# Kernel tuning notes

Hardware: AMD Instinct MI355X
Metric: run time of the kernel (lower is better)

## Reference

```python
import jax, jax.numpy as jnp
import numpy as np

EMBED_DIM = 512
NUM_HEADS = 8
HEAD_DIM = EMBED_DIM // NUM_HEADS
SHIFT_INIT = 5.0
EPS = 1e-6


def setup_inputs() -> dict:
    key = jax.random.key(0)
    ks = jax.random.split(key, 8)
    L, N, E = 2048, 4, EMBED_DIM
    query = jax.random.normal(ks[0], (L, N, E), dtype=jnp.float32)
    k_in = jax.random.normal(ks[1], (L, N, E), dtype=jnp.float32)
    v_in = jax.random.normal(ks[2], (L, N, E), dtype=jnp.float32)
    # MultiheadAttention packed projections
    in_proj_weight = jax.random.normal(ks[3], (3 * E, E), dtype=jnp.float32) / np.sqrt(E)
    in_proj_bias = jnp.zeros((3 * E,), dtype=jnp.float32)
    out_proj_weight = jax.random.normal(ks[4], (E, E), dtype=jnp.float32) / np.sqrt(E)
    out_proj_bias = jnp.zeros((E,), dtype=jnp.float32)
    # GeM parameters: p ~ N(1, 0.02), shift = 5
    p = 1.0 + 0.02 * jax.random.normal(ks[5], (E,), dtype=jnp.float32)
    shift = jnp.full((E,), SHIFT_INIT, dtype=jnp.float32)
    return {
        "query": query, "key": k_in, "value": v_in,
        "in_proj_weight": in_proj_weight, "in_proj_bias": in_proj_bias,
        "out_proj_weight": out_proj_weight, "out_proj_bias": out_proj_bias,
        "p": p, "shift": shift,
    }


def reference(query, key, value, in_proj_weight, in_proj_bias,
              out_proj_weight, out_proj_bias, p, shift):
    L, N, E = query.shape
    H, D = NUM_HEADS, HEAD_DIM
    w_q, w_k, w_v = jnp.split(in_proj_weight, 3, axis=0)   # each (E, E)
    b_q, b_k, b_v = jnp.split(in_proj_bias, 3, axis=0)

    def proj(x, w, b):
        # (L, N, E) -> (N, H, L, D)
        y = x @ w.T + b
        return y.reshape(L, N, H, D).transpose(1, 2, 0, 3)

    q = proj(query, w_q, b_q)
    k = proj(key, w_k, b_k)
    v = proj(value, w_v, b_v)

    scale = 1.0 / np.sqrt(D)
    scores = jnp.einsum('nhld,nhsd->nhls', q, k) * scale   # (N,H,L,S)
    attn = jax.nn.softmax(scores, axis=-1)

    # GeM pooling of values: shift -> power p -> weighted mean -> inverse power -> unshift
    p_h = p.reshape(H, D)[None, :, None, :]                # (1,H,1,D)
    shift_h = shift.reshape(H, D)[None, :, None, :]
    v_pos = jnp.maximum(v + shift_h, EPS)                  # keep base positive
    pooled = jnp.einsum('nhls,nhsd->nhld', attn, v_pos ** p_h)
    out_h = jnp.maximum(pooled, EPS) ** (1.0 / p_h) - shift_h  # (N,H,L,D)

    out = out_h.transpose(2, 0, 1, 3).reshape(L, N, E)     # back to (L,N,E)
    out = out @ out_proj_weight.T + out_proj_bias
    return out
```

## Files before the change

kernel.cpp:

```cpp
#include <hip/hip_runtime.h>
#include <hip/hip_bf16.h>

#define E_DIM 512
#define N_BATCH 4
#define L_SEQ 2048
#define N_HEADS 8
#define H_DIM 64
#define N_ROWS (L_SEQ * N_BATCH)
#define EPS_F 1e-6f
#define SC_Q 0.18033688f

typedef __attribute__((ext_vector_type(8))) short bf16x8;
typedef __attribute__((ext_vector_type(8))) _Float16 f16x8;
typedef __attribute__((ext_vector_type(4))) float f32x4;
typedef __attribute__((ext_vector_type(16))) float f32x16;

__device__ __forceinline__ void split2(float f, __hip_bfloat16& h, __hip_bfloat16& l) {
  h = __float2bfloat16(f);
  l = __float2bfloat16(f - __bfloat162float(h));
}

__device__ __forceinline__ unsigned int packf16(float a, float b) {
  union { _Float16 h[2]; unsigned int u; } c;
  c.h[0] = (_Float16)a;
  c.h[1] = (_Float16)b;
  return c.u;
}

__global__ __launch_bounds__(256) void wconv_kernel(
    const float* __restrict__ wio, const float* __restrict__ wo,
    __hip_bfloat16* __restrict__ wiohi, __hip_bfloat16* __restrict__ wiolo,
    __hip_bfloat16* __restrict__ wohi, __hip_bfloat16* __restrict__ wolo) {
  const int g = blockIdx.x * 256 + threadIdx.x;
  const float* src;
  __hip_bfloat16 *dh, *dl;
  int i;
  if (g < 196608) { src = wio; dh = wiohi; dl = wiolo; i = g * 4; }
  else            { src = wo;  dh = wohi;  dl = wolo;  i = (g - 196608) * 4; }
  const float4 f = *(const float4*)(src + i);
  alignas(8) __hip_bfloat16 h[4], l[4];
  split2(f.x, h[0], l[0]); split2(f.y, h[1], l[1]);
  split2(f.z, h[2], l[2]); split2(f.w, h[3], l[3]);
  *(uint2*)(dh + i) = *(const uint2*)h;
  *(uint2*)(dl + i) = *(const uint2*)l;
}

__global__ __launch_bounds__(256, 3) void proj_qkv_kernel(
    const float* __restrict__ xq, const float* __restrict__ xk,
    const float* __restrict__ xv, const __hip_bfloat16* __restrict__ whi,
    const float* __restrict__ bias, const float* __restrict__ pw,
    const float* __restrict__ sw,
    _Float16* __restrict__ qbuf, _Float16* __restrict__ kbuf,
    float* __restrict__ ubuf) {
  __shared__ __hip_bfloat16 Xh[128][40];
  __shared__ __hip_bfloat16 Xl[128][40];
  __shared__ __hip_bfloat16 Wh[128][40];
  const int z = blockIdx.z;
  const int row0 = blockIdx.x * 128;
  const int col0 = blockIdx.y * 128;
  const float* __restrict__ xsrc = (z == 0) ? xq : (z == 1) ? xk : xv;
  const int tid = threadIdx.x;
  const int lane = tid & 63;
  const int wv = tid >> 6;
  const int lidx = lane & 15;
  const int quad = lane >> 4;
  const int srow = tid >> 1;
  const int scol = (tid & 1) * 16;

  f32x4 acc[2][8];
#pragma unroll
  for (int rt = 0; rt < 2; ++rt)
#pragma unroll
    for (int ct = 0; ct < 8; ++ct) acc[rt][ct] = (f32x4){0.f, 0.f, 0.f, 0.f};

  const int ar0 = wv * 32 + lidx;

  for (int kt = 0; kt < 16; ++kt) {
    const int k0 = kt * 32;
    {
      const float* xp = xsrc + (size_t)(row0 + srow) * E_DIM + k0 + scol;
      float f[16];
      *(float4*)&f[0]  = ((const float4*)xp)[0];
      *(float4*)&f[4]  = ((const float4*)xp)[1];
      *(float4*)&f[8]  = ((const float4*)xp)[2];
      *(float4*)&f[12] = ((const float4*)xp)[3];
      alignas(16) __hip_bfloat16 hi[16], lo[16];
#pragma unroll
      for (int j = 0; j < 16; ++j) split2(f[j], hi[j], lo[j]);
      *(uint4*)&Xh[srow][scol]     = ((const uint4*)hi)[0];
      *(uint4*)&Xh[srow][scol + 8] = ((const uint4*)hi)[1];
      *(uint4*)&Xl[srow][scol]     = ((const uint4*)lo)[0];
      *(uint4*)&Xl[srow][scol + 8] = ((const uint4*)lo)[1];
    }
    {
      const size_t wof = (size_t)(z * E_DIM + col0 + srow) * E_DIM + k0 + scol;
      *(uint4*)&Wh[srow][scol]     = ((const uint4*)(whi + wof))[0];
      *(uint4*)&Wh[srow][scol + 8] = ((const uint4*)(whi + wof))[1];
    }
    __syncthreads();

    const bf16x8 ah0 = *(const bf16x8*)&Xh[ar0][quad * 8];
    const bf16x8 ah1 = *(const bf16x8*)&Xh[ar0 + 16][quad * 8];
    const bf16x8 al0 = *(const bf16x8*)&Xl[ar0][quad * 8];
    const bf16x8 al1 = *(const bf16x8*)&Xl[ar0 + 16][quad * 8];
#pragma unroll
    for (int ct = 0; ct < 8; ++ct) {
      const bf16x8 bh = *(const bf16x8*)&Wh[ct * 16 + lidx][quad * 8];
      acc[0][ct] = __builtin_amdgcn_mfma_f32_16x16x32_bf16(ah0, bh, acc[0][ct], 0, 0, 0);
      acc[0][ct] = __builtin_amdgcn_mfma_f32_16x16x32_bf16(al0, bh, acc[0][ct], 0, 0, 0);
      acc[1][ct] = __builtin_amdgcn_mfma_f32_16x16x32_bf16(ah1, bh, acc[1][ct], 0, 0, 0);
      acc[1][ct] = __builtin_amdgcn_mfma_f32_16x16x32_bf16(al1, bh, acc[1][ct], 0, 0, 0);
    }
    __syncthreads();
  }

  if (z < 2) {
    _Float16* __restrict__ dst = (z == 0) ? qbuf : kbuf;
    const float scale = (z == 0) ? SC_Q : 1.0f;
    float bv[8];
#pragma unroll
    for (int ct = 0; ct < 8; ++ct) bv[ct] = bias[z * E_DIM + col0 + ct * 16 + lidx];
#pragma unroll
    for (int rt = 0; rt < 2; ++rt)
#pragma unroll
      for (int ct = 0; ct < 8; ++ct) {
        const int e = col0 + ct * 16 + lidx;
        const int h = e >> 6, d = e & 63;
#pragma unroll
        for (int reg = 0; reg < 4; ++reg) {
          const int R = row0 + wv * 32 + rt * 16 + quad * 4 + reg;
          const int lpos = R >> 2, nb = R & 3;
          dst[(((size_t)nb * N_HEADS + h) * L_SEQ + lpos) * H_DIM + d] =
              (_Float16)((acc[rt][ct][reg] + bv[ct]) * scale);
        }
      }
  } else {
    float bv[8], pv[8], sv[8];
#pragma unroll
    for (int ct = 0; ct < 8; ++ct) {
      const int e = col0 + ct * 16 + lidx;
      bv[ct] = bias[2 * E_DIM + e]; pv[ct] = pw[e]; sv[ct] = sw[e];
    }
#pragma unroll
    for (int rt = 0; rt < 2; ++rt)
#pragma unroll
      for (int ct = 0; ct < 8; ++ct) {
        const int e = col0 + ct * 16 + lidx;
        const int h = e >> 6, d = e & 63;
#pragma unroll
        for (int reg = 0; reg < 4; ++reg) {
          const int R = row0 + wv * 32 + rt * 16 + quad * 4 + reg;
          const int lpos = R >> 2, nb = R & 3;
          const float y = acc[rt][ct][reg] + bv[ct];
          const float vp = fmaxf(y + sv[ct], EPS_F);
          ubuf[(((size_t)nb * N_HEADS + h) * L_SEQ + lpos) * H_DIM + d] =
              __powf(vp, pv[ct]);
        }
      }
  }
}

__global__ __launch_bounds__(256) void transp_kernel(
    const float* __restrict__ u, _Float16* __restrict__ uT) {
  __shared__ float T[64][65];
  const int lt = blockIdx.x, h = blockIdx.y, nb = blockIdx.z;
  const int tid = threadIdx.x;
  const int r = tid >> 2;
  const int cb = (tid & 3) * 16;
  const size_t srcbase = ((size_t)nb * N_HEADS + h) * L_SEQ + lt * 64;
  {
    const float* p = u + (srcbase + r) * H_DIM + cb;
    *(float4*)&T[r][cb + 0]  = ((const float4*)p)[0];
    *(float4*)&T[r][cb + 4]  = ((const float4*)p)[1];
    *(float4*)&T[r][cb + 8]  = ((const float4*)p)[2];
    *(float4*)&T[r][cb + 12] = ((const float4*)p)[3];
  }
  __syncthreads();
  alignas(16) _Float16 hv[16];
#pragma unroll
  for (int j = 0; j < 16; ++j) hv[j] = (_Float16)T[cb + j][r];
  const size_t dst = (((size_t)nb * N_HEADS + h) * H_DIM + r) * L_SEQ + lt * 64 + cb;
  *(uint4*)(uT + dst)     = ((const uint4*)hv)[0];
  *(uint4*)(uT + dst + 8) = ((const uint4*)hv)[1];
}

__global__ __launch_bounds__(256, 4) void attn_kernel(
    const _Float16* __restrict__ qbuf, const _Float16* __restrict__ kbuf,
    const _Float16* __restrict__ uT, const float* __restrict__ pw,
    const float* __restrict__ sw, __hip_bfloat16* __restrict__ ohhi,
    __hip_bfloat16* __restrict__ ohlo) {
  __shared__ union {
    struct { _Float16 Ks[128][72]; _Float16 Us[64][136]; } st;
    struct { float A[2][64][32]; float lA[2][64]; } red;
  } sm;
  const int qt = blockIdx.x, h = blockIdx.y, nb = blockIdx.z;
  const int q0 = qt * 64;
  const int tid = threadIdx.x;
  const int lane = tid & 63;
  const int w = tid >> 6;
  const int wv = w & 1;
  const int sg = w >> 1;
  const int lm = lane & 31;
  const int kg = lane >> 5;
  const int srow = tid >> 1;
  const int scb = (tid & 1) * 32;
  const int urow = tid >> 2;
  const int ucb = (tid & 3) * 32;
  const size_t headbase = ((size_t)nb * N_HEADS + h) * L_SEQ;
  const size_t dbase = ((size_t)nb * N_HEADS + h) * H_DIM;

  f16x8 bq[4];
#pragma unroll
  for (int kc = 0; kc < 4; ++kc)
    bq[kc] = *(const f16x8*)(qbuf +
        (headbase + q0 + wv * 32 + lm) * H_DIM + kc * 16 + kg * 8);

  f32x16 o[2];
  o[0] = (f32x16)(0.f); o[1] = (f32x16)(0.f);
  float lsum = 0.f;

  for (int it = 0; it < 16; ++it) {
    const int s0 = it * 128;
    __syncthreads();
    {
      const _Float16* kp = kbuf + (headbase + s0 + srow) * H_DIM + scb;
      *(uint4*)&sm.st.Ks[srow][scb + 0]  = ((const uint4*)kp)[0];
      *(uint4*)&sm.st.Ks[srow][scb + 8]  = ((const uint4*)kp)[1];
      *(uint4*)&sm.st.Ks[srow][scb + 16] = ((const uint4*)kp)[2];
      *(uint4*)&sm.st.Ks[srow][scb + 24] = ((const uint4*)kp)[3];
      const _Float16* up = uT + (dbase + urow) * L_SEQ + s0 + ucb;
      *(uint4*)&sm.st.Us[urow][ucb + 0]  = ((const uint4*)up)[0];
      *(uint4*)&sm.st.Us[urow][ucb + 8]  = ((const uint4*)up)[1];
      *(uint4*)&sm.st.Us[urow][ucb + 16] = ((const uint4*)up)[2];
      *(uint4*)&sm.st.Us[urow][ucb + 24] = ((const uint4*)up)[3];
    }
    __syncthreads();

    const int sr = sg * 64;

    f32x16 sc[2];
    sc[0] = (f32x16)(0.f); sc[1] = (f32x16)(0.f);
#pragma unroll
    for (int kc = 0; kc < 4; ++kc) {
      const f16x8 ak0 = *(const f16x8*)&sm.st.Ks[sr + lm][kc * 16 + kg * 8];
      const f16x8 ak1 = *(const f16x8*)&sm.st.Ks[sr + 32 + lm][kc * 16 + kg * 8];
      sc[0] = __builtin_amdgcn_mfma_f32_32x32x16_f16(ak0, bq[kc], sc[0], 0, 0, 0);
      sc[1] = __builtin_amdgcn_mfma_f32_32x32x16_f16(ak1, bq[kc], sc[1], 0, 0, 0);
    }

    unsigned int P2[2][4][2];
#pragma unroll
    for (int mt = 0; mt < 2; ++mt)
#pragma unroll
      for (int g = 0; g < 4; ++g) {
        const float p0 = __builtin_amdgcn_exp2f(sc[mt][4 * g + 0]);
        const float p1 = __builtin_amdgcn_exp2f(sc[mt][4 * g + 1]);
        const float p2 = __builtin_amdgcn_exp2f(sc[mt][4 * g + 2]);
        const float p3 = __builtin_amdgcn_exp2f(sc[mt][4 * g + 3]);
        lsum += (p0 + p1) + (p2 + p3);
        P2[mt][g][0] = packf16(p0, p1);
        P2[mt][g][1] = packf16(p2, p3);
      }

#pragma unroll
    for (int kc = 0; kc < 4; ++kc) {
      const int mt = kc >> 1;
      const f16x8 au0 = *(const f16x8*)&sm.st.Us[lm][sr + kc * 16 + kg * 8];
      const f16x8 au1 = *(const f16x8*)&sm.st.Us[32 + lm][sr + kc * 16 + kg * 8];
      const int gx = (2 * kc) & 3, gy = (2 * kc + 1) & 3;
      const unsigned int x0 = P2[mt][gx][0], x1 = P2[mt][gx][1];
      const unsigned int y0 = P2[mt][gy][0], y1 = P2[mt][gy][1];
      const unsigned int sA = kg ? x0 : y0, sB = kg ? x1 : y1;
      const unsigned int rA = (unsigned int)__shfl_xor((int)sA, 32);
      const unsigned int rB = (unsigned int)__shfl_xor((int)sB, 32);
      union { unsigned int u[4]; f16x8 v; } bp;
      bp.u[0] = kg ? rA : x0;
      bp.u[1] = kg ? rB : x1;
      bp.u[2] = kg ? y0 : rA;
      bp.u[3] = kg ? y1 : rB;
      o[0] = __builtin_amdgcn_mfma_f32_32x32x16_f16(au0, bp.v, o[0], 0, 0, 0);
      o[1] = __builtin_amdgcn_mfma_f32_32x32x16_f16(au1, bp.v, o[1], 0, 0, 0);
    }
  }

  float* redA = &sm.red.A[0][0][0];
  float* lrA = &sm.red.lA[0][0];

  __syncthreads();
  if (sg == 1) {
    lrA[wv * 64 + lane] = lsum;
#pragma unroll
    for (int mt2 = 0; mt2 < 2; ++mt2)
#pragma unroll
      for (int g = 0; g < 4; ++g) {
        const int i4 = (mt2 * 4 + g) ^ (lane & 7);
        float4 v = {o[mt2][4 * g + 0], o[mt2][4 * g + 1],
                    o[mt2][4 * g + 2], o[mt2][4 * g + 3]};
        *(float4*)(redA + ((size_t)(wv * 64 + lane)) * 32 + i4 * 4) = v;
      }
  }
  __syncthreads();
  if (sg == 1) return;
  lsum += lrA[wv * 64 + lane];
#pragma unroll
  for (int mt2 = 0; mt2 < 2; ++mt2)
#pragma unroll
    for (int g = 0; g < 4; ++g) {
      const int i4 = (mt2 * 4 + g) ^ (lane & 7);
      const float4 v =
          *(const float4*)(redA + ((size_t)(wv * 64 + lane)) * 32 + i4 * 4);
      o[mt2][4 * g + 0] += v.x; o[mt2][4 * g + 1] += v.y;
      o[mt2][4 * g + 2] += v.z; o[mt2][4 * g + 3] += v.w;
    }

  {
    const float l = lsum + __shfl_xor(lsum, 32);
    const float inv = 1.0f / l;
    const int qg = q0 + wv * 32 + lm;
    const size_t base = ((size_t)qg * N_BATCH + nb) * E_DIM + h * H_DIM;
#pragma unroll
    for (int mt2 = 0; mt2 < 2; ++mt2)
#pragma unroll
      for (int g = 0; g < 4; ++g) {
        alignas(8) __hip_bfloat16 hb[4], lb[4];
#pragma unroll
        for (int i = 0; i < 4; ++i) {
          const int d = mt2 * 32 + 8 * g + 4 * kg + i;
          const int e = h * H_DIM + d;
          const float pooled = o[mt2][4 * g + i] * inv;
          const float val = __powf(fmaxf(pooled, EPS_F), 1.0f / pw[e]) - sw[e];
          split2(val, hb[i], lb[i]);
        }
        const int d0 = mt2 * 32 + 8 * g + 4 * kg;
        *(uint2*)(ohhi + base + d0) = *(const uint2*)hb;
        *(uint2*)(ohlo + base + d0) = *(const uint2*)lb;
      }
  }
}

__global__ __launch_bounds__(256, 4) void out_proj_kernel(
    const __hip_bfloat16* __restrict__ xhi, const __hip_bfloat16* __restrict__ xlo,
    const __hip_bfloat16* __restrict__ whi, const __hip_bfloat16* __restrict__ wlo,
    const float* __restrict__ bias, float* __restrict__ out) {
  __shared__ __hip_bfloat16 Xh[128][40];
  __shared__ __hip_bfloat16 Xl[128][40];
  __shared__ __hip_bfloat16 Wh[64][40];
  __shared__ __hip_bfloat16 Wl[64][40];
  const int row0 = blockIdx.x * 128;
  const int col0 = blockIdx.y * 64;
  const int tid = threadIdx.x;
  const int lane = tid & 63;
  const int wv = tid >> 6;
  const int lidx = lane & 15;
  const int quad = lane >> 4;
  const int srow = tid >> 1;
  const int scol = (tid & 1) * 16;
  const int wrow = tid >> 2;
  const int wcol = (tid & 3) * 8;

  f32x4 acc[2][4];
#pragma unroll
  for (int rt = 0; rt < 2; ++rt)
#pragma unroll
    for (int ct = 0; ct < 4; ++ct) acc[rt][ct] = (f32x4){0.f, 0.f, 0.f, 0.f};

  const int ar0 = wv * 32 + lidx;

  for (int kt = 0; kt < 16; ++kt) {
    const int k0 = kt * 32;
    {
      const size_t xof = (size_t)(row0 + srow) * E_DIM + k0 + scol;
      *(uint4*)&Xh[srow][scol]     = ((const uint4*)(xhi + xof))[0];
      *(uint4*)&Xh[srow][scol + 8] = ((const uint4*)(xhi + xof))[1];
      *(uint4*)&Xl[srow][scol]     = ((const uint4*)(xlo + xof))[0];
      *(uint4*)&Xl[srow][scol + 8] = ((const uint4*)(xlo + xof))[1];
      const size_t wof = (size_t)(col0 + wrow) * E_DIM + k0 + wcol;
      *(uint4*)&Wh[wrow][wcol] = *(const uint4*)(whi + wof);
      *(uint4*)&Wl[wrow][wcol] = *(const uint4*)(wlo + wof);
    }
    __syncthreads();

    const bf16x8 ah0 = *(const bf16x8*)&Xh[ar0][quad * 8];
    const bf16x8 ah1 = *(const bf16x8*)&Xh[ar0 + 16][quad * 8];
    const bf16x8 al0 = *(const bf16x8*)&Xl[ar0][quad * 8];
    const bf16x8 al1 = *(const bf16x8*)&Xl[ar0 + 16][quad * 8];
#pragma unroll
    for (int ct = 0; ct < 4; ++ct) {
      const bf16x8 bh = *(const bf16x8*)&Wh[ct * 16 + lidx][quad * 8];
      const bf16x8 bl = *(const bf16x8*)&Wl[ct * 16 + lidx][quad * 8];
      acc[0][ct] = __builtin_amdgcn_mfma_f32_16x16x32_bf16(ah0, bh, acc[0][ct], 0, 0, 0);
      acc[0][ct] = __builtin_amdgcn_mfma_f32_16x16x32_bf16(al0, bh, acc[0][ct], 0, 0, 0);
      acc[0][ct] = __builtin_amdgcn_mfma_f32_16x16x32_bf16(ah0, bl, acc[0][ct], 0, 0, 0);
      acc[1][ct] = __builtin_amdgcn_mfma_f32_16x16x32_bf16(ah1, bh, acc[1][ct], 0, 0, 0);
      acc[1][ct] = __builtin_amdgcn_mfma_f32_16x16x32_bf16(al1, bh, acc[1][ct], 0, 0, 0);
      acc[1][ct] = __builtin_amdgcn_mfma_f32_16x16x32_bf16(ah1, bl, acc[1][ct], 0, 0, 0);
    }
    __syncthreads();
  }

  float bv[4];
#pragma unroll
  for (int ct = 0; ct < 4; ++ct) bv[ct] = bias[col0 + ct * 16 + lidx];
#pragma unroll
  for (int rt = 0; rt < 2; ++rt)
#pragma unroll
    for (int ct = 0; ct < 4; ++ct) {
      const int c = col0 + ct * 16 + lidx;
#pragma unroll
      for (int reg = 0; reg < 4; ++reg) {
        const int R = row0 + wv * 32 + rt * 16 + quad * 4 + reg;
        out[(size_t)R * E_DIM + c] = acc[rt][ct][reg] + bv[ct];
      }
    }
}

extern "C" void kernel_launch(void* const* d_in, const int* in_sizes, int n_in,
                              void* d_out, int out_size, void* d_ws, size_t ws_size,
                              hipStream_t stream) {
  const float* q_in = (const float*)d_in[0];
  const float* k_in = (const float*)d_in[1];
  const float* v_in = (const float*)d_in[2];
  const float* wio  = (const float*)d_in[3];
  const float* bio  = (const float*)d_in[4];
  const float* wo   = (const float*)d_in[5];
  const float* bo   = (const float*)d_in[6];
  const float* pw   = (const float*)d_in[7];
  const float* sw   = (const float*)d_in[8];

  const size_t NE = (size_t)N_ROWS * E_DIM;
  _Float16* qbuf = (_Float16*)d_ws;
  _Float16* kbuf = qbuf + NE;
  float* ubuf = (float*)(kbuf + NE);
  _Float16* uT = (_Float16*)(ubuf + NE);
  __hip_bfloat16* wiohi = (__hip_bfloat16*)(uT + NE);
  __hip_bfloat16* wiolo = wiohi + 786432;
  __hip_bfloat16* wohi  = wiolo + 786432;
  __hip_bfloat16* wolo  = wohi + 262144;
  __hip_bfloat16* ohhi = (__hip_bfloat16*)ubuf;
  __hip_bfloat16* ohlo = ohhi + NE;

  wconv_kernel<<<dim3(1024), 256, 0, stream>>>(wio, wo, wiohi, wiolo, wohi, wolo);
  proj_qkv_kernel<<<dim3(64, 4, 3), 256, 0, stream>>>(q_in, k_in, v_in, wiohi,
                                                      bio, pw, sw, qbuf, kbuf, ubuf);
  transp_kernel<<<dim3(32, 8, 4), 256, 0, stream>>>(ubuf, uT);
  attn_kernel<<<dim3(32, 8, 4), 256, 0, stream>>>(qbuf, kbuf, uT, pw, sw,
                                                  ohhi, ohlo);
  out_proj_kernel<<<dim3(64, 8), 256, 0, stream>>>(ohhi, ohlo, wohi, wolo,
                                                   bo, (float*)d_out);
}
```

Measured before the change: 294.9 us.

## Restructure attention to per-wave direct global loads with XCD-aware block mapping

The attention kernel drops its LDS staging and split-K cross-wave reduction. Each wave now owns 32 queries and streams K and U fragments straight from global memory (L2) in 64-key steps. Blocks are remapped so that heads are grouped per XCD, and the occupancy hint is lowered. The kernel also adds s_setprio around MFMA bursts and replaces the shuffle-and-select with v_permlane32_swap. Separately, the powered values are stored as fp16 instead of fp32 before the transpose, halving that intermediate traffic. The cost is more global and L2 load pressure and less inter-wave data reuse.

Result: slower. 420.9 us (+42.7%).

```diff
diff --git a/kernel.cpp b/kernel.cpp
--- a/kernel.cpp
+++ b/kernel.cpp
@@ -51,7 +51,7 @@
     const float* __restrict__ bias, const float* __restrict__ pw,
     const float* __restrict__ sw,
     _Float16* __restrict__ qbuf, _Float16* __restrict__ kbuf,
-    float* __restrict__ ubuf) {
+    _Float16* __restrict__ ubuf) {
   __shared__ __hip_bfloat16 Xh[128][40];
   __shared__ __hip_bfloat16 Xl[128][40];
   __shared__ __hip_bfloat16 Wh[128][40];
@@ -154,58 +154,51 @@
           const float y = acc[rt][ct][reg] + bv[ct];
           const float vp = fmaxf(y + sv[ct], EPS_F);
           ubuf[(((size_t)nb * N_HEADS + h) * L_SEQ + lpos) * H_DIM + d] =
-              __powf(vp, pv[ct]);
+              (_Float16)__powf(vp, pv[ct]);
         }
       }
   }
 }
 
 __global__ __launch_bounds__(256) void transp_kernel(
-    const float* __restrict__ u, _Float16* __restrict__ uT) {
-  __shared__ float T[64][65];
+    const _Float16* __restrict__ u, _Float16* __restrict__ uT) {
+  __shared__ _Float16 T[64][72];
   const int lt = blockIdx.x, h = blockIdx.y, nb = blockIdx.z;
   const int tid = threadIdx.x;
   const int r = tid >> 2;
   const int cb = (tid & 3) * 16;
   const size_t srcbase = ((size_t)nb * N_HEADS + h) * L_SEQ + lt * 64;
   {
-    const float* p = u + (srcbase + r) * H_DIM + cb;
-    *(float4*)&T[r][cb + 0]  = ((const float4*)p)[0];
-    *(float4*)&T[r][cb + 4]  = ((const float4*)p)[1];
-    *(float4*)&T[r][cb + 8]  = ((const float4*)p)[2];
-    *(float4*)&T[r][cb + 12] = ((const float4*)p)[3];
+    const _Float16* p = u + (srcbase + r) * H_DIM + cb;
+    *(uint4*)&T[r][cb + 0] = ((const uint4*)p)[0];
+    *(uint4*)&T[r][cb + 8] = ((const uint4*)p)[1];
   }
   __syncthreads();
   alignas(16) _Float16 hv[16];
 #pragma unroll
-  for (int j = 0; j < 16; ++j) hv[j] = (_Float16)T[cb + j][r];
+  for (int j = 0; j < 16; ++j) hv[j] = T[cb + j][r];
   const size_t dst = (((size_t)nb * N_HEADS + h) * H_DIM + r) * L_SEQ + lt * 64 + cb;
   *(uint4*)(uT + dst)     = ((const uint4*)hv)[0];
   *(uint4*)(uT + dst + 8) = ((const uint4*)hv)[1];
 }
 
-__global__ __launch_bounds__(256, 4) void attn_kernel(
+__global__ __launch_bounds__(256, 2) void attn_kernel(
     const _Float16* __restrict__ qbuf, const _Float16* __restrict__ kbuf,
     const _Float16* __restrict__ uT, const float* __restrict__ pw,
     const float* __restrict__ sw, __hip_bfloat16* __restrict__ ohhi,
     __hip_bfloat16* __restrict__ ohlo) {
-  __shared__ union {
-    struct { _Float16 Ks[128][72]; _Float16 Us[64][136]; } st;
-    struct { float A[2][64][32]; float lA[2][64]; } red;
-  } sm;
-  const int qt = blockIdx.x, h = blockIdx.y, nb = blockIdx.z;
-  const int q0 = qt * 64;
+  const int f = blockIdx.x;
+  const int xcd = f & 7;
+  const int j = f >> 3;
+  const int qt = j & 15;
+  const int hidx = xcd * 4 + (j >> 4);
+  const int h = hidx & 7, nb = hidx >> 3;
   const int tid = threadIdx.x;
   const int lane = tid & 63;
   const int w = tid >> 6;
-  const int wv = w & 1;
-  const int sg = w >> 1;
+  const int q0 = qt * 128 + w * 32;
   const int lm = lane & 31;
   const int kg = lane >> 5;
-  const int srow = tid >> 1;
-  const int scb = (tid & 1) * 32;
-  const int urow = tid >> 2;
-  const int ucb = (tid & 3) * 32;
   const size_t headbase = ((size_t)nb * N_HEADS + h) * L_SEQ;
   const size_t dbase = ((size_t)nb * N_HEADS + h) * H_DIM;
 
@@ -213,110 +206,77 @@
 #pragma unroll
   for (int kc = 0; kc < 4; ++kc)
     bq[kc] = *(const f16x8*)(qbuf +
-        (headbase + q0 + wv * 32 + lm) * H_DIM + kc * 16 + kg * 8);
+        (headbase + q0 + lm) * H_DIM + kc * 16 + kg * 8);
 
   f32x16 o[2];
   o[0] = (f32x16)(0.f); o[1] = (f32x16)(0.f);
   float lsum = 0.f;
 
-  for (int it = 0; it < 16; ++it) {
-    const int s0 = it * 128;
-    __syncthreads();
-    {
-      const _Float16* kp = kbuf + (headbase + s0 + srow) * H_DIM + scb;
-      *(uint4*)&sm.st.Ks[srow][scb + 0]  = ((const uint4*)kp)[0];
-      *(uint4*)&sm.st.Ks[srow][scb + 8]  = ((const uint4*)kp)[1];
-      *(uint4*)&sm.st.Ks[srow][scb + 16] = ((const uint4*)kp)[2];
-      *(uint4*)&sm.st.Ks[srow][scb + 24] = ((const uint4*)kp)[3];
-      const _Float16* up = uT + (dbase + urow) * L_SEQ + s0 + ucb;
-      *(uint4*)&sm.st.Us[urow][ucb + 0]  = ((const uint4*)up)[0];
-      *(uint4*)&sm.st.Us[urow][ucb + 8]  = ((const uint4*)up)[1];
-      *(uint4*)&sm.st.Us[urow][ucb + 16] = ((const uint4*)up)[2];
-      *(uint4*)&sm.st.Us[urow][ucb + 24] = ((const uint4*)up)[3];
-    }
-    __syncthreads();
-
-    const int sr = sg * 64;
-
-    f32x16 sc[2];
-    sc[0] = (f32x16)(0.f); sc[1] = (f32x16)(0.f);
+  const _Float16* __restrict__ kp0 = kbuf + (headbase + lm) * H_DIM;
+  const _Float16* __restrict__ kp1 = kbuf + (headbase + 32 + lm) * H_DIM;
+  const _Float16* __restrict__ up0 = uT + (dbase + lm) * L_SEQ;
+  const _Float16* __restrict__ up1 = uT + (dbase + 32 + lm) * L_SEQ;
+
+  for (int s0 = 0; s0 < L_SEQ; s0 += 64) {
+    f16x8 ak0[4], ak1[4], au0[4], au1[4];
 #pragma unroll
     for (int kc = 0; kc < 4; ++kc) {
-      const f16x8 ak0 = *(const f16x8*)&sm.st.Ks[sr + lm][kc * 16 + kg * 8];
-      const f16x8 ak1 = *(const f16x8*)&sm.st.Ks[sr + 32 + lm][kc * 16 + kg * 8];
-      sc[0] = __builtin_amdgcn_mfma_f32_32x32x16_f16(ak0, bq[kc], sc[0], 0, 0, 0);
-      sc[1] = __builtin_amdgcn_mfma_f32_32x32x16_f16(ak1, bq[kc], sc[1], 0, 0, 0);
-    }
+      const int c = kc * 16 + kg * 8;
+      ak0[kc] = *(const f16x8*)(kp0 + (size_t)s0 * H_DIM + c);
+      ak1[kc] = *(const f16x8*)(kp1 + (size_t)s0 * H_DIM + c);
+      au0[kc] = *(const f16x8*)(up0 + s0 + c);
+      au1[kc] = *(const f16x8*)(up1 + s0 + c);
+    }
+
+    f32x16 sc0 = (f32x16)(0.f), sc1 = (f32x16)(0.f);
+    __builtin_amdgcn_s_setprio(1);
+#pragma unroll
+    for (int kc = 0; kc < 4; ++kc) {
+      sc0 = __builtin_amdgcn_mfma_f32_32x32x16_f16(ak0[kc], bq[kc], sc0, 0, 0, 0);
+      sc1 = __builtin_amdgcn_mfma_f32_32x32x16_f16(ak1[kc], bq[kc], sc1, 0, 0, 0);
+    }
+    __builtin_amdgcn_s_setprio(0);
 
     unsigned int P2[2][4][2];
 #pragma unroll
-    for (int mt = 0; mt < 2; ++mt)
+    for (int mt = 0; mt < 2; ++mt) {
+      const f32x16& sc = mt ? sc1 : sc0;
 #pragma unroll
       for (int g = 0; g < 4; ++g) {
-        const float p0 = __builtin_amdgcn_exp2f(sc[mt][4 * g + 0]);
-        const float p1 = __builtin_amdgcn_exp2f(sc[mt][4 * g + 1]);
-        const float p2 = __builtin_amdgcn_exp2f(sc[mt][4 * g + 2]);
-        const float p3 = __builtin_amdgcn_exp2f(sc[mt][4 * g + 3]);
+        const float p0 = __builtin_amdgcn_exp2f(sc[4 * g + 0]);
+        const float p1 = __builtin_amdgcn_exp2f(sc[4 * g + 1]);
+        const float p2 = __builtin_amdgcn_exp2f(sc[4 * g + 2]);
+        const float p3 = __builtin_amdgcn_exp2f(sc[4 * g + 3]);
         lsum += (p0 + p1) + (p2 + p3);
         P2[mt][g][0] = packf16(p0, p1);
         P2[mt][g][1] = packf16(p2, p3);
       }
-
+    }
+
+    __builtin_amdgcn_s_setprio(1);
 #pragma unroll
     for (int kc = 0; kc < 4; ++kc) {
       const int mt = kc >> 1;
-      const f16x8 au0 = *(const f16x8*)&sm.st.Us[lm][sr + kc * 16 + kg * 8];
-      const f16x8 au1 = *(const f16x8*)&sm.st.Us[32 + lm][sr + kc * 16 + kg * 8];
       const int gx = (2 * kc) & 3, gy = (2 * kc + 1) & 3;
-      const unsigned int x0 = P2[mt][gx][0], x1 = P2[mt][gx][1];
-      const unsigned int y0 = P2[mt][gy][0], y1 = P2[mt][gy][1];
-      const unsigned int sA = kg ? x0 : y0, sB = kg ? x1 : y1;
-      const unsigned int rA = (unsigned int)__shfl_xor((int)sA, 32);
-      const unsigned int rB = (unsigned int)__shfl_xor((int)sB, 32);
+      unsigned int a0 = P2[mt][gx][0], b0 = P2[mt][gy][0];
+      unsigned int a1 = P2[mt][gx][1], b1 = P2[mt][gy][1];
+      asm("v_permlane32_swap_b32 %0, %1" : "+v"(a0), "+v"(b0));
+      asm("v_permlane32_swap_b32 %0, %1" : "+v"(a1), "+v"(b1));
       union { unsigned int u[4]; f16x8 v; } bp;
-      bp.u[0] = kg ? rA : x0;
-      bp.u[1] = kg ? rB : x1;
-      bp.u[2] = kg ? y0 : rA;
-      bp.u[3] = kg ? y1 : rB;
-      o[0] = __builtin_amdgcn_mfma_f32_32x32x16_f16(au0, bp.v, o[0], 0, 0, 0);
-      o[1] = __builtin_amdgcn_mfma_f32_32x32x16_f16(au1, bp.v, o[1], 0, 0, 0);
-    }
-  }
-
-  float* redA = &sm.red.A[0][0][0];
-  float* lrA = &sm.red.lA[0][0];
-
-  __syncthreads();
-  if (sg == 1) {
-    lrA[wv * 64 + lane] = lsum;
-#pragma unroll
-    for (int mt2 = 0; mt2 < 2; ++mt2)
-#pragma unroll
-      for (int g = 0; g < 4; ++g) {
-        const int i4 = (mt2 * 4 + g) ^ (lane & 7);
-        float4 v = {o[mt2][4 * g + 0], o[mt2][4 * g + 1],
-                    o[mt2][4 * g + 2], o[mt2][4 * g + 3]};
-        *(float4*)(redA + ((size_t)(wv * 64 + lane)) * 32 + i4 * 4) = v;
-      }
-  }
-  __syncthreads();
-  if (sg == 1) return;
-  lsum += lrA[wv * 64 + lane];
-#pragma unroll
-  for (int mt2 = 0; mt2 < 2; ++mt2)
-#pragma unroll
-    for (int g = 0; g < 4; ++g) {
-      const int i4 = (mt2 * 4 + g) ^ (lane & 7);
-      const float4 v =
-          *(const float4*)(redA + ((size_t)(wv * 64 + lane)) * 32 + i4 * 4);
-      o[mt2][4 * g + 0] += v.x; o[mt2][4 * g + 1] += v.y;
-      o[mt2][4 * g + 2] += v.z; o[mt2][4 * g + 3] += v.w;
-    }
+      bp.u[0] = a0;
+      bp.u[1] = a1;
+      bp.u[2] = b0;
+      bp.u[3] = b1;
+      o[0] = __builtin_amdgcn_mfma_f32_32x32x16_f16(au0[kc], bp.v, o[0], 0, 0, 0);
+      o[1] = __builtin_amdgcn_mfma_f32_32x32x16_f16(au1[kc], bp.v, o[1], 0, 0, 0);
+    }
+    __builtin_amdgcn_s_setprio(0);
+  }
 
   {
     const float l = lsum + __shfl_xor(lsum, 32);
     const float inv = 1.0f / l;
-    const int qg = q0 + wv * 32 + lm;
+    const int qg = q0 + lm;
     const size_t base = ((size_t)qg * N_BATCH + nb) * E_DIM + h * H_DIM;
 #pragma unroll
     for (int mt2 = 0; mt2 < 2; ++mt2)
@@ -441,10 +401,11 @@
 
   wconv_kernel<<<dim3(1024), 256, 0, stream>>>(wio, wo, wiohi, wiolo, wohi, wolo);
   proj_qkv_kernel<<<dim3(64, 4, 3), 256, 0, stream>>>(q_in, k_in, v_in, wiohi,
-                                                      bio, pw, sw, qbuf, kbuf, ubuf);
-  transp_kernel<<<dim3(32, 8, 4), 256, 0, stream>>>(ubuf, uT);
-  attn_kernel<<<dim3(32, 8, 4), 256, 0, stream>>>(qbuf, kbuf, uT, pw, sw,
-                                                  ohhi, ohlo);
+                                                      bio, pw, sw, qbuf, kbuf,
+                                                      (_Float16*)ubuf);
+  transp_kernel<<<dim3(32, 8, 4), 256, 0, stream>>>((const _Float16*)ubuf, uT);
+  attn_kernel<<<dim3(512), 256, 0, stream>>>(qbuf, kbuf, uT, pw, sw,
+                                             ohhi, ohlo);
   out_proj_kernel<<<dim3(64, 8), 256, 0, stream>>>(ohhi, ohlo, wohi, wolo,
                                                    bo, (float*)d_out);
 }
```
